# Optimization experiments

Measured on AMD Instinct MI355X. Metric: run time of the kernel, lower is better.

The kernel has to match this reference:

```python
import jax, jax.numpy as jnp
import numpy as np
import math

HIDDEN = 256
HEADS = 8
HEAD_DIM = HIDDEN // HEADS
SCALE = math.sqrt(HEAD_DIM)


def setup_inputs() -> dict:
    key = jax.random.key(0)
    ks = jax.random.split(key, 10)
    B, N = 2, 4096
    x = jax.random.normal(ks[0], (B, N, HIDDEN), dtype=jnp.float32)
    pos = jax.random.normal(ks[1], (B, N, 3), dtype=jnp.float32)
    s = 1.0 / math.sqrt(HIDDEN)
    Wq = jax.random.normal(ks[2], (HIDDEN, HIDDEN), dtype=jnp.float32) * s
    bq = jnp.zeros((HIDDEN,), dtype=jnp.float32)
    Wk = jax.random.normal(ks[3], (HIDDEN, HIDDEN), dtype=jnp.float32) * s
    bk = jnp.zeros((HIDDEN,), dtype=jnp.float32)
    Wv = jax.random.normal(ks[4], (HIDDEN, HIDDEN), dtype=jnp.float32) * s
    bv = jnp.zeros((HIDDEN,), dtype=jnp.float32)
    Wo = jax.random.normal(ks[5], (HIDDEN, HIDDEN), dtype=jnp.float32) * s
    bo = jnp.zeros((HIDDEN,), dtype=jnp.float32)
    return {"x": x, "pos": pos, "Wq": Wq, "bq": bq, "Wk": Wk, "bk": bk,
            "Wv": Wv, "bv": bv, "Wo": Wo, "bo": bo}


def _pairwise_dist(pos):
    # Euclidean cdist via the norm trick; clip for numerical safety.
    sq = jnp.sum(pos * pos, axis=-1)  # [B, N]
    d2 = sq[:, :, None] + sq[:, None, :] - 2.0 * jnp.einsum('bic,bjc->bij', pos, pos)
    return jnp.sqrt(jnp.maximum(d2, 0.0))  # [B, N, N]


def reference(x, pos, Wq, bq, Wk, bk, Wv, bv, Wo, bo):
    B, N, _ = x.shape
    # projections -> [B, H, N, Dh]
    def split_heads(t):
        return t.reshape(B, N, HEADS, HEAD_DIM).transpose(0, 2, 1, 3)
    q = split_heads(x @ Wq.T + bq)
    k = split_heads(x @ Wk.T + bk)
    v = split_heads(x @ Wv.T + bv)
    scores = jnp.einsum('bhid,bhjd->bhij', q, k) / SCALE
    dist_bias = -_pairwise_dist(pos) / 10.0  # [B, N, N]
    scores = scores + dist_bias[:, None, :, :]
    attn = jax.nn.softmax(scores, axis=-1)
    out = jnp.einsum('bhij,bhjd->bhid', attn, v)
    out = out.transpose(0, 2, 1, 3).reshape(B, N, HIDDEN)
    return out @ Wo.T + bo
```

## Files before the change

kernel.cpp:

```cpp
#include <hip/hip_runtime.h>

#define BATCH 2
#define SEQ   4096
#define HID   256
#define NHEAD 8
#define DH    32

typedef __attribute__((ext_vector_type(8))) _Float16 half8;
typedef __attribute__((ext_vector_type(4))) _Float16 half4;
typedef __attribute__((ext_vector_type(4))) float    f32x4;

__global__ void cvt_f32_f16(const float* __restrict__ src,
                            _Float16* __restrict__ dst, int n) {
    int i = (blockIdx.x * blockDim.x + threadIdx.x) * 4;
    if (i >= n) return;
    f32x4 v = *reinterpret_cast<const f32x4*>(src + i);
    half4 h;
#pragma unroll
    for (int c = 0; c < 4; ++c) h[c] = (_Float16)v[c];
    *reinterpret_cast<half4*>(dst + i) = h;
}

__global__ __launch_bounds__(256) void qkv_proj(
    const _Float16* __restrict__ xh, const _Float16* __restrict__ Wh,
    const float* __restrict__ bq, const float* __restrict__ bk,
    const float* __restrict__ bv,
    _Float16* __restrict__ Qh, _Float16* __restrict__ Kh,
    _Float16* __restrict__ Vt)
{
    const int z   = blockIdx.z;
    const int m0  = blockIdx.x * 64;
    const int n0  = blockIdx.y * 64;
    const int tid = threadIdx.x;
    const int w   = tid >> 6, lane = tid & 63;
    const int lr  = lane & 15, lg = lane >> 4;
    const int wr  = (w >> 1) * 32, wc = (w & 1) * 32;

    const _Float16* Wp = Wh + (size_t)z * HID * HID;
    const float* bias = (z == 0) ? bq : (z == 1) ? bk : bv;

    f32x4 acc[2][2] = {};
    const int ar = m0 + wr + lr;
    const int br = n0 + wc + lr;
#pragma unroll
    for (int ks = 0; ks < 8; ++ks) {
        const int ko = ks * 32 + lg * 8;
        half8 a0 = *reinterpret_cast<const half8*>(xh + (size_t)ar * HID + ko);
        half8 a1 = *reinterpret_cast<const half8*>(xh + (size_t)(ar + 16) * HID + ko);
        half8 b0 = *reinterpret_cast<const half8*>(Wp + (size_t)br * HID + ko);
        half8 b1 = *reinterpret_cast<const half8*>(Wp + (size_t)(br + 16) * HID + ko);
        acc[0][0] = __builtin_amdgcn_mfma_f32_16x16x32_f16(a0, b0, acc[0][0], 0, 0, 0);
        acc[0][1] = __builtin_amdgcn_mfma_f32_16x16x32_f16(a0, b1, acc[0][1], 0, 0, 0);
        acc[1][0] = __builtin_amdgcn_mfma_f32_16x16x32_f16(a1, b0, acc[1][0], 0, 0, 0);
        acc[1][1] = __builtin_amdgcn_mfma_f32_16x16x32_f16(a1, b1, acc[1][1], 0, 0, 0);
    }
#pragma unroll
    for (int mf = 0; mf < 2; ++mf)
#pragma unroll
    for (int nf = 0; nf < 2; ++nf)
#pragma unroll
    for (int r = 0; r < 4; ++r) {
        const int m  = m0 + wr + mf * 16 + lg * 4 + r;
        const int o  = n0 + wc + nf * 16 + lr;
        const int bb = m >> 12, nn = m & (SEQ - 1);
        const int hh = o >> 5,  dd = o & (DH - 1);
        float v = acc[mf][nf][r] + bias[o];
        if (z == 0) {
            Qh[(((size_t)(bb * NHEAD + hh) * SEQ) + nn) * DH + dd] =
                (_Float16)(v * 0.17677669529663687f);
        } else if (z == 1) {
            Kh[(((size_t)(bb * NHEAD + hh) * SEQ) + nn) * DH + dd] = (_Float16)v;
        } else {
            Vt[(((size_t)(bb * NHEAD + hh) * DH) + dd) * SEQ + nn] = (_Float16)v;
        }
    }
}

__global__ __launch_bounds__(512) void attn_kernel(
    const _Float16* __restrict__ Qh, const _Float16* __restrict__ Kh,
    const _Float16* __restrict__ Vt, const float* __restrict__ pos,
    _Float16* __restrict__ AO)
{
    __shared__ __align__(16) float pi[32][4];
    __shared__ __align__(16) float pj[64][4];
    __shared__ __align__(16) float sbias[32][68];
    __shared__ __align__(16) _Float16 Pl[NHEAD][2048];

    const int b   = blockIdx.y;
    const int i0  = blockIdx.x * 32;
    const int tid = threadIdx.x;
    const int h   = tid >> 6;
    const int lane = tid & 63;
    const int lr  = lane & 15, lg = lane >> 4;

    if (tid < 32) {
        const float* p = pos + (size_t)(b * SEQ + i0 + tid) * 3;
        float x = p[0], y = p[1], zz = p[2];
        pi[tid][0] = x; pi[tid][1] = y; pi[tid][2] = zz;
        pi[tid][3] = x * x + y * y + zz * zz;
    }

    const _Float16* Qbase = Qh + ((size_t)(b * NHEAD + h) * SEQ + i0) * DH;
    const _Float16* Kbase = Kh + (size_t)(b * NHEAD + h) * SEQ * DH;
    const _Float16* Vbase = Vt + (size_t)(b * NHEAD + h) * DH * SEQ;

    const half8 aq0 = *reinterpret_cast<const half8*>(Qbase + (size_t)lr * DH + lg * 8);
    const half8 aq1 = *reinterpret_cast<const half8*>(Qbase + (size_t)(16 + lr) * DH + lg * 8);

    f32x4 acc[2][2] = {};
    float mrun[2][4], lrun[2][4];
#pragma unroll
    for (int mf = 0; mf < 2; ++mf)
#pragma unroll
    for (int r = 0; r < 4; ++r) { mrun[mf][r] = -__builtin_inff(); lrun[mf][r] = 0.f; }

    char* Pbytes = (char*)&Pl[h][0];

    for (int jt = 0; jt < SEQ / 64; ++jt) {
        const int j0 = jt * 64;
        __syncthreads();
        if (tid < 64) {
            const float* p = pos + (size_t)(b * SEQ + j0 + tid) * 3;
            float x = p[0], y = p[1], zz = p[2];
            pj[tid][0] = x; pj[tid][1] = y; pj[tid][2] = zz;
            pj[tid][3] = x * x + y * y + zz * zz;
        }
        __syncthreads();
        {
            const int row = tid >> 4, c0 = (tid & 15) * 4;
            const float xi = pi[row][0], yi = pi[row][1], zi = pi[row][2], si = pi[row][3];
            f32x4 bb;
#pragma unroll
            for (int c = 0; c < 4; ++c) {
                const int col = c0 + c;
                float dot = xi * pj[col][0] + yi * pj[col][1] + zi * pj[col][2];
                float d2  = si + pj[col][3] - 2.f * dot;
                bb[c] = -0.1f * sqrtf(fmaxf(d2, 0.f));
            }
            *reinterpret_cast<f32x4*>(&sbias[row][c0]) = bb;
        }
        __syncthreads();

        half8 bk8[4];
#pragma unroll
        for (int cf = 0; cf < 4; ++cf)
            bk8[cf] = *reinterpret_cast<const half8*>(
                Kbase + (size_t)(j0 + cf * 16 + lr) * DH + lg * 8);
        f32x4 s[2][4];
#pragma unroll
        for (int mf = 0; mf < 2; ++mf)
#pragma unroll
        for (int cf = 0; cf < 4; ++cf) {
            f32x4 zero = {};
            s[mf][cf] = __builtin_amdgcn_mfma_f32_16x16x32_f16(
                mf ? aq1 : aq0, bk8[cf], zero, 0, 0, 0);
        }

#pragma unroll
        for (int mf = 0; mf < 2; ++mf)
#pragma unroll
        for (int r = 0; r < 4; ++r) {
            const int row = mf * 16 + lg * 4 + r;
            float v[4];
#pragma unroll
            for (int c = 0; c < 4; ++c) v[c] = s[mf][c][r] + sbias[row][c * 16 + lr];
            float tmax = fmaxf(fmaxf(v[0], v[1]), fmaxf(v[2], v[3]));
#pragma unroll
            for (int msk = 8; msk >= 1; msk >>= 1)
                tmax = fmaxf(tmax, __shfl_xor(tmax, msk, 64));
            const float mold = mrun[mf][r];
            const float mnew = fmaxf(mold, tmax);
            const float alpha = __expf(mold - mnew);
            float rsum = 0.f;
#pragma unroll
            for (int c = 0; c < 4; ++c) { v[c] = __expf(v[c] - mnew); rsum += v[c]; }
#pragma unroll
            for (int msk = 8; msk >= 1; msk >>= 1)
                rsum += __shfl_xor(rsum, msk, 64);
            lrun[mf][r] = lrun[mf][r] * alpha + rsum;
            mrun[mf][r] = mnew;
            acc[mf][0][r] *= alpha;
            acc[mf][1][r] *= alpha;
#pragma unroll
            for (int c = 0; c < 4; ++c) {
                const int col = c * 16 + lr;
                const int off = (row * 128 + col * 2) ^ ((row & 7) << 4);
                *reinterpret_cast<_Float16*>(Pbytes + off) = (_Float16)v[c];
            }
        }

#pragma unroll
        for (int ks = 0; ks < 2; ++ks) {
            half8 bv0 = *reinterpret_cast<const half8*>(
                Vbase + (size_t)lr * SEQ + j0 + ks * 32 + lg * 8);
            half8 bv1 = *reinterpret_cast<const half8*>(
                Vbase + (size_t)(16 + lr) * SEQ + j0 + ks * 32 + lg * 8);
#pragma unroll
            for (int mf = 0; mf < 2; ++mf) {
                const int prow = mf * 16 + lr;
                const int poff = (prow * 128 + (ks * 32 + lg * 8) * 2) ^ ((prow & 7) << 4);
                half8 pa = *reinterpret_cast<const half8*>(Pbytes + poff);
                acc[mf][0] = __builtin_amdgcn_mfma_f32_16x16x32_f16(pa, bv0, acc[mf][0], 0, 0, 0);
                acc[mf][1] = __builtin_amdgcn_mfma_f32_16x16x32_f16(pa, bv1, acc[mf][1], 0, 0, 0);
            }
        }
    }

#pragma unroll
    for (int mf = 0; mf < 2; ++mf)
#pragma unroll
    for (int r = 0; r < 4; ++r) {
        const float inv = 1.f / lrun[mf][r];
        const int row = mf * 16 + lg * 4 + r;
#pragma unroll
        for (int df = 0; df < 2; ++df) {
            AO[((size_t)(b * SEQ + i0 + row)) * HID + h * DH + df * 16 + lr] =
                (_Float16)(acc[mf][df][r] * inv);
        }
    }
}

__global__ __launch_bounds__(256) void out_proj(
    const _Float16* __restrict__ AO, const _Float16* __restrict__ Woh,
    const float* __restrict__ bo, float* __restrict__ out)
{
    const int m0  = blockIdx.x * 64;
    const int n0  = blockIdx.y * 64;
    const int tid = threadIdx.x;
    const int w   = tid >> 6, lane = tid & 63;
    const int lr  = lane & 15, lg = lane >> 4;
    const int wr  = (w >> 1) * 32, wc = (w & 1) * 32;

    f32x4 acc[2][2] = {};
    const int ar = m0 + wr + lr;
    const int br = n0 + wc + lr;
#pragma unroll
    for (int ks = 0; ks < 8; ++ks) {
        const int ko = ks * 32 + lg * 8;
        half8 a0 = *reinterpret_cast<const half8*>(AO + (size_t)ar * HID + ko);
        half8 a1 = *reinterpret_cast<const half8*>(AO + (size_t)(ar + 16) * HID + ko);
        half8 b0 = *reinterpret_cast<const half8*>(Woh + (size_t)br * HID + ko);
        half8 b1 = *reinterpret_cast<const half8*>(Woh + (size_t)(br + 16) * HID + ko);
        acc[0][0] = __builtin_amdgcn_mfma_f32_16x16x32_f16(a0, b0, acc[0][0], 0, 0, 0);
        acc[0][1] = __builtin_amdgcn_mfma_f32_16x16x32_f16(a0, b1, acc[0][1], 0, 0, 0);
        acc[1][0] = __builtin_amdgcn_mfma_f32_16x16x32_f16(a1, b0, acc[1][0], 0, 0, 0);
        acc[1][1] = __builtin_amdgcn_mfma_f32_16x16x32_f16(a1, b1, acc[1][1], 0, 0, 0);
    }
#pragma unroll
    for (int mf = 0; mf < 2; ++mf)
#pragma unroll
    for (int nf = 0; nf < 2; ++nf)
#pragma unroll
    for (int r = 0; r < 4; ++r) {
        const int m = m0 + wr + mf * 16 + lg * 4 + r;
        const int o = n0 + wc + nf * 16 + lr;
        out[(size_t)m * HID + o] = acc[mf][nf][r] + bo[o];
    }
}

extern "C" void kernel_launch(void* const* d_in, const int* in_sizes, int n_in,
                              void* d_out, int out_size, void* d_ws, size_t ws_size,
                              hipStream_t stream)
{
    const float* x   = (const float*)d_in[0];
    const float* pos = (const float*)d_in[1];
    const float* Wq  = (const float*)d_in[2];
    const float* bq  = (const float*)d_in[3];
    const float* Wk  = (const float*)d_in[4];
    const float* bk  = (const float*)d_in[5];
    const float* Wv  = (const float*)d_in[6];
    const float* bv  = (const float*)d_in[7];
    const float* Wo  = (const float*)d_in[8];
    const float* bo  = (const float*)d_in[9];
    float* out = (float*)d_out;

    char* ws = (char*)d_ws;
    _Float16* Qh = (_Float16*)(ws);
    _Float16* Kh = (_Float16*)(ws + (4  << 20));
    _Float16* Vt = (_Float16*)(ws + (8  << 20));
    _Float16* xh = (_Float16*)(ws + (12 << 20));
    _Float16* AO = xh;
    _Float16* Wh = (_Float16*)(ws + (16 << 20));

    const int NX = BATCH * SEQ * HID;
    const int NW = HID * HID;
    cvt_f32_f16<<<NX / 1024, 256, 0, stream>>>(x,  xh, NX);
    cvt_f32_f16<<<NW / 1024, 256, 0, stream>>>(Wq, Wh + 0 * NW, NW);
    cvt_f32_f16<<<NW / 1024, 256, 0, stream>>>(Wk, Wh + 1 * NW, NW);
    cvt_f32_f16<<<NW / 1024, 256, 0, stream>>>(Wv, Wh + 2 * NW, NW);
    cvt_f32_f16<<<NW / 1024, 256, 0, stream>>>(Wo, Wh + 3 * NW, NW);

    qkv_proj<<<dim3(BATCH * SEQ / 64, HID / 64, 3), 256, 0, stream>>>(
        xh, Wh, bq, bk, bv, Qh, Kh, Vt);

    attn_kernel<<<dim3(SEQ / 32, BATCH), 512, 0, stream>>>(Qh, Kh, Vt, pos, AO);

    out_proj<<<dim3(BATCH * SEQ / 64, HID / 64), 256, 0, stream>>>(
        AO, Wh + 3 * NW, bo, out);
}
```

Before: 287.8 us.

## Restructure attention: 16-row tiles, exp2 softmax, lazy rescale, fused weight conversion

Rewrites the attention kernel to handle 16 query rows per block and compute the distance bias in 256-column chunks, which cuts the number of block-wide barriers. Softmax switches to exp2 by folding log2(e) into the Q scale and the bias constant, and uses transposed MFMA output so each lane reduces within its own registers. The running max is rescaled only when a tile's max exceeds it by a threshold, skipping most rescales. The four weight conversions are fused into one launch. The tradeoffs are that the bias is now recomputed per 16-row block rather than per 32-row block, and the lazy rescale lets unnormalized values grow up to 2^11.5 before fp16 conversion.

Measured after the change: 235.7 us. 18.1% less time.

```diff
diff --git a/kernel.cpp b/kernel.cpp
--- a/kernel.cpp
+++ b/kernel.cpp
@@ -5,6 +5,9 @@
 #define HID   256
 #define NHEAD 8
 #define DH    32
+#define THR_L2 11.5f
+#define QSCALE 0.25501639769925074f
+#define BIASC (-0.14426950408889634f)
 
 typedef __attribute__((ext_vector_type(8))) _Float16 half8;
 typedef __attribute__((ext_vector_type(4))) _Float16 half4;
@@ -19,6 +22,19 @@
 #pragma unroll
     for (int c = 0; c < 4; ++c) h[c] = (_Float16)v[c];
     *reinterpret_cast<half4*>(dst + i) = h;
+}
+
+__global__ void cvt_w4(const float* __restrict__ a, const float* __restrict__ b,
+                       const float* __restrict__ c, const float* __restrict__ d,
+                       _Float16* __restrict__ dst) {
+    const float* srcs[4] = {a, b, c, d};
+    const float* s = srcs[blockIdx.y];
+    const int i = (blockIdx.x * blockDim.x + threadIdx.x) * 4;
+    f32x4 v = *reinterpret_cast<const f32x4*>(s + i);
+    half4 h;
+#pragma unroll
+    for (int k = 0; k < 4; ++k) h[k] = (_Float16)v[k];
+    *reinterpret_cast<half4*>(dst + (size_t)blockIdx.y * HID * HID + i) = h;
 }
 
 __global__ __launch_bounds__(256) void qkv_proj(
@@ -67,7 +83,7 @@
         float v = acc[mf][nf][r] + bias[o];
         if (z == 0) {
             Qh[(((size_t)(bb * NHEAD + hh) * SEQ) + nn) * DH + dd] =
-                (_Float16)(v * 0.17677669529663687f);
+                (_Float16)(v * QSCALE);
         } else if (z == 1) {
             Kh[(((size_t)(bb * NHEAD + hh) * SEQ) + nn) * DH + dd] = (_Float16)v;
         } else {
@@ -76,147 +92,146 @@
     }
 }
 
-__global__ __launch_bounds__(512) void attn_kernel(
+__global__ __launch_bounds__(512, 4) void attn_kernel(
     const _Float16* __restrict__ Qh, const _Float16* __restrict__ Kh,
     const _Float16* __restrict__ Vt, const float* __restrict__ pos,
     _Float16* __restrict__ AO)
 {
-    __shared__ __align__(16) float pi[32][4];
-    __shared__ __align__(16) float pj[64][4];
-    __shared__ __align__(16) float sbias[32][68];
-    __shared__ __align__(16) _Float16 Pl[NHEAD][2048];
-
-    const int b   = blockIdx.y;
-    const int i0  = blockIdx.x * 32;
-    const int tid = threadIdx.x;
-    const int h   = tid >> 6;
+    __shared__ __align__(16) float pi4[16][4];
+    __shared__ __align__(16) float pj4[256][4];
+    __shared__ __align__(16) float biasL[16][260];
+    __shared__ __align__(16) _Float16 Pl[NHEAD][16 * 72];
+    __shared__ __align__(16) float xposeL[NHEAD][16];
+
+    const int b    = blockIdx.y;
+    const int i0   = blockIdx.x * 16;
+    const int tid  = threadIdx.x;
+    const int w    = tid >> 6;
     const int lane = tid & 63;
-    const int lr  = lane & 15, lg = lane >> 4;
-
-    if (tid < 32) {
+    const int lr   = lane & 15, lg = lane >> 4;
+
+    if (tid < 16) {
         const float* p = pos + (size_t)(b * SEQ + i0 + tid) * 3;
-        float x = p[0], y = p[1], zz = p[2];
-        pi[tid][0] = x; pi[tid][1] = y; pi[tid][2] = zz;
-        pi[tid][3] = x * x + y * y + zz * zz;
-    }
-
-    const _Float16* Qbase = Qh + ((size_t)(b * NHEAD + h) * SEQ + i0) * DH;
-    const _Float16* Kbase = Kh + (size_t)(b * NHEAD + h) * SEQ * DH;
-    const _Float16* Vbase = Vt + (size_t)(b * NHEAD + h) * DH * SEQ;
-
-    const half8 aq0 = *reinterpret_cast<const half8*>(Qbase + (size_t)lr * DH + lg * 8);
-    const half8 aq1 = *reinterpret_cast<const half8*>(Qbase + (size_t)(16 + lr) * DH + lg * 8);
-
-    f32x4 acc[2][2] = {};
-    float mrun[2][4], lrun[2][4];
-#pragma unroll
-    for (int mf = 0; mf < 2; ++mf)
-#pragma unroll
-    for (int r = 0; r < 4; ++r) { mrun[mf][r] = -__builtin_inff(); lrun[mf][r] = 0.f; }
-
-    char* Pbytes = (char*)&Pl[h][0];
-
-    for (int jt = 0; jt < SEQ / 64; ++jt) {
-        const int j0 = jt * 64;
+        float x = p[0], y = p[1], z = p[2];
+        pi4[tid][0] = x; pi4[tid][1] = y; pi4[tid][2] = z;
+        pi4[tid][3] = x * x + y * y + z * z;
+    }
+
+    const size_t bhh = (size_t)(b * NHEAD + w);
+    const _Float16* Qbase = Qh + (bhh * SEQ + i0) * DH;
+    const _Float16* Kbase = Kh + bhh * SEQ * DH;
+    const _Float16* Vbase = Vt + bhh * DH * SEQ;
+
+    const half8 aq = *reinterpret_cast<const half8*>(Qbase + (size_t)lr * DH + lg * 8);
+
+    f32x4 acc0 = {}, acc1 = {};
+    float mrun = -1e30f, lsum = 0.f;
+
+    char* PlW = (char*)&Pl[w][0];
+
+    for (int ch = 0; ch < SEQ / 256; ++ch) {
         __syncthreads();
-        if (tid < 64) {
-            const float* p = pos + (size_t)(b * SEQ + j0 + tid) * 3;
-            float x = p[0], y = p[1], zz = p[2];
-            pj[tid][0] = x; pj[tid][1] = y; pj[tid][2] = zz;
-            pj[tid][3] = x * x + y * y + zz * zz;
+        if (tid < 256) {
+            const float* p = pos + (size_t)(b * SEQ + ch * 256 + tid) * 3;
+            float x = p[0], y = p[1], z = p[2];
+            pj4[tid][0] = x; pj4[tid][1] = y; pj4[tid][2] = z;
+            pj4[tid][3] = x * x + y * y + z * z;
         }
         __syncthreads();
         {
-            const int row = tid >> 4, c0 = (tid & 15) * 4;
-            const float xi = pi[row][0], yi = pi[row][1], zi = pi[row][2], si = pi[row][3];
-            f32x4 bb;
-#pragma unroll
-            for (int c = 0; c < 4; ++c) {
-                const int col = c0 + c;
-                float dot = xi * pj[col][0] + yi * pj[col][1] + zi * pj[col][2];
-                float d2  = si + pj[col][3] - 2.f * dot;
-                bb[c] = -0.1f * sqrtf(fmaxf(d2, 0.f));
-            }
-            *reinterpret_cast<f32x4*>(&sbias[row][c0]) = bb;
+            const int br  = tid & 15;
+            const int c0  = (tid >> 4) * 8;
+            const float xi = pi4[br][0], yi = pi4[br][1], zi = pi4[br][2], si = pi4[br][3];
+            f32x4 o0, o1;
+#pragma unroll
+            for (int k = 0; k < 8; ++k) {
+                const float* pj = &pj4[c0 + k][0];
+                float dot = xi * pj[0] + yi * pj[1] + zi * pj[2];
+                float d2  = si + pj[3] - 2.f * dot;
+                float v   = BIASC * sqrtf(fmaxf(d2, 0.f));
+                if (k < 4) o0[k] = v; else o1[k - 4] = v;
+            }
+            *reinterpret_cast<f32x4*>(&biasL[br][c0])     = o0;
+            *reinterpret_cast<f32x4*>(&biasL[br][c0 + 4]) = o1;
         }
         __syncthreads();
 
-        half8 bk8[4];
-#pragma unroll
-        for (int cf = 0; cf < 4; ++cf)
-            bk8[cf] = *reinterpret_cast<const half8*>(
-                Kbase + (size_t)(j0 + cf * 16 + lr) * DH + lg * 8);
-        f32x4 s[2][4];
-#pragma unroll
-        for (int mf = 0; mf < 2; ++mf)
-#pragma unroll
-        for (int cf = 0; cf < 4; ++cf) {
-            f32x4 zero = {};
-            s[mf][cf] = __builtin_amdgcn_mfma_f32_16x16x32_f16(
-                mf ? aq1 : aq0, bk8[cf], zero, 0, 0, 0);
+        for (int s = 0; s < 4; ++s) {
+            const int j0 = ch * 256 + s * 64;
+
+            half8 k8[4];
+#pragma unroll
+            for (int cf = 0; cf < 4; ++cf)
+                k8[cf] = *reinterpret_cast<const half8*>(
+                    Kbase + (size_t)(j0 + cf * 16 + lr) * DH + lg * 8);
+
+            f32x4 vv[4];
+#pragma unroll
+            for (int cf = 0; cf < 4; ++cf) {
+                f32x4 zero = {};
+                f32x4 sv = __builtin_amdgcn_mfma_f32_16x16x32_f16(k8[cf], aq, zero, 0, 0, 0);
+                f32x4 bb = *reinterpret_cast<const f32x4*>(
+                    &biasL[lr][s * 64 + cf * 16 + lg * 4]);
+                vv[cf] = sv + bb;
+            }
+
+            float tmax = vv[0][0];
+#pragma unroll
+            for (int cf = 0; cf < 4; ++cf)
+#pragma unroll
+            for (int t = 0; t < 4; ++t) tmax = fmaxf(tmax, vv[cf][t]);
+
+            if (!__all(tmax <= mrun + THR_L2)) {
+                float tm = tmax;
+                tm = fmaxf(tm, __shfl_xor(tm, 16, 64));
+                tm = fmaxf(tm, __shfl_xor(tm, 32, 64));
+                const float mnew  = fmaxf(mrun, tm);
+                const float alpha = exp2f(mrun - mnew);
+                if (lane < 16) xposeL[w][lane] = alpha;
+                f32x4 a4 = *reinterpret_cast<const f32x4*>(&xposeL[w][lg * 4]);
+                lsum *= alpha;
+                mrun = mnew;
+                acc0 *= a4;
+                acc1 *= a4;
+            }
+
+#pragma unroll
+            for (int cf = 0; cf < 4; ++cf) {
+                f32x4 p;
+#pragma unroll
+                for (int t = 0; t < 4; ++t) p[t] = exp2f(vv[cf][t] - mrun);
+                lsum += (p[0] + p[1]) + (p[2] + p[3]);
+                half4 hp;
+#pragma unroll
+                for (int t = 0; t < 4; ++t) hp[t] = (_Float16)p[t];
+                *reinterpret_cast<half4*>(
+                    PlW + lr * 144 + (cf * 16 + lg * 4) * 2) = hp;
+            }
+
+#pragma unroll
+            for (int ks = 0; ks < 2; ++ks) {
+                half8 pa = *reinterpret_cast<const half8*>(
+                    PlW + lr * 144 + (ks * 32 + lg * 8) * 2);
+                half8 bv0 = *reinterpret_cast<const half8*>(
+                    Vbase + (size_t)lr * SEQ + j0 + ks * 32 + lg * 8);
+                half8 bv1 = *reinterpret_cast<const half8*>(
+                    Vbase + (size_t)(16 + lr) * SEQ + j0 + ks * 32 + lg * 8);
+                acc0 = __builtin_amdgcn_mfma_f32_16x16x32_f16(pa, bv0, acc0, 0, 0, 0);
+                acc1 = __builtin_amdgcn_mfma_f32_16x16x32_f16(pa, bv1, acc1, 0, 0, 0);
+            }
         }
-
-#pragma unroll
-        for (int mf = 0; mf < 2; ++mf)
-#pragma unroll
-        for (int r = 0; r < 4; ++r) {
-            const int row = mf * 16 + lg * 4 + r;
-            float v[4];
-#pragma unroll
-            for (int c = 0; c < 4; ++c) v[c] = s[mf][c][r] + sbias[row][c * 16 + lr];
-            float tmax = fmaxf(fmaxf(v[0], v[1]), fmaxf(v[2], v[3]));
-#pragma unroll
-            for (int msk = 8; msk >= 1; msk >>= 1)
-                tmax = fmaxf(tmax, __shfl_xor(tmax, msk, 64));
-            const float mold = mrun[mf][r];
-            const float mnew = fmaxf(mold, tmax);
-            const float alpha = __expf(mold - mnew);
-            float rsum = 0.f;
-#pragma unroll
-            for (int c = 0; c < 4; ++c) { v[c] = __expf(v[c] - mnew); rsum += v[c]; }
-#pragma unroll
-            for (int msk = 8; msk >= 1; msk >>= 1)
-                rsum += __shfl_xor(rsum, msk, 64);
-            lrun[mf][r] = lrun[mf][r] * alpha + rsum;
-            mrun[mf][r] = mnew;
-            acc[mf][0][r] *= alpha;
-            acc[mf][1][r] *= alpha;
-#pragma unroll
-            for (int c = 0; c < 4; ++c) {
-                const int col = c * 16 + lr;
-                const int off = (row * 128 + col * 2) ^ ((row & 7) << 4);
-                *reinterpret_cast<_Float16*>(Pbytes + off) = (_Float16)v[c];
-            }
-        }
-
-#pragma unroll
-        for (int ks = 0; ks < 2; ++ks) {
-            half8 bv0 = *reinterpret_cast<const half8*>(
-                Vbase + (size_t)lr * SEQ + j0 + ks * 32 + lg * 8);
-            half8 bv1 = *reinterpret_cast<const half8*>(
-                Vbase + (size_t)(16 + lr) * SEQ + j0 + ks * 32 + lg * 8);
-#pragma unroll
-            for (int mf = 0; mf < 2; ++mf) {
-                const int prow = mf * 16 + lr;
-                const int poff = (prow * 128 + (ks * 32 + lg * 8) * 2) ^ ((prow & 7) << 4);
-                half8 pa = *reinterpret_cast<const half8*>(Pbytes + poff);
-                acc[mf][0] = __builtin_amdgcn_mfma_f32_16x16x32_f16(pa, bv0, acc[mf][0], 0, 0, 0);
-                acc[mf][1] = __builtin_amdgcn_mfma_f32_16x16x32_f16(pa, bv1, acc[mf][1], 0, 0, 0);
-            }
-        }
-    }
-
-#pragma unroll
-    for (int mf = 0; mf < 2; ++mf)
-#pragma unroll
-    for (int r = 0; r < 4; ++r) {
-        const float inv = 1.f / lrun[mf][r];
-        const int row = mf * 16 + lg * 4 + r;
-#pragma unroll
-        for (int df = 0; df < 2; ++df) {
-            AO[((size_t)(b * SEQ + i0 + row)) * HID + h * DH + df * 16 + lr] =
-                (_Float16)(acc[mf][df][r] * inv);
-        }
+    }
+
+    lsum += __shfl_xor(lsum, 16, 64);
+    lsum += __shfl_xor(lsum, 32, 64);
+    const float inv = 1.f / lsum;
+    if (lane < 16) xposeL[w][lane] = inv;
+    f32x4 i4 = *reinterpret_cast<const f32x4*>(&xposeL[w][lg * 4]);
+#pragma unroll
+    for (int t = 0; t < 4; ++t) {
+        const size_t row = (size_t)(b * SEQ + i0 + lg * 4 + t) * HID + w * DH;
+        AO[row + lr]      = (_Float16)(acc0[t] * i4[t]);
+        AO[row + 16 + lr] = (_Float16)(acc1[t] * i4[t]);
     }
 }
 
@@ -284,16 +299,13 @@
 
     const int NX = BATCH * SEQ * HID;
     const int NW = HID * HID;
-    cvt_f32_f16<<<NX / 1024, 256, 0, stream>>>(x,  xh, NX);
-    cvt_f32_f16<<<NW / 1024, 256, 0, stream>>>(Wq, Wh + 0 * NW, NW);
-    cvt_f32_f16<<<NW / 1024, 256, 0, stream>>>(Wk, Wh + 1 * NW, NW);
-    cvt_f32_f16<<<NW / 1024, 256, 0, stream>>>(Wv, Wh + 2 * NW, NW);
-    cvt_f32_f16<<<NW / 1024, 256, 0, stream>>>(Wo, Wh + 3 * NW, NW);
+    cvt_f32_f16<<<NX / 1024, 256, 0, stream>>>(x, xh, NX);
+    cvt_w4<<<dim3(NW / 1024, 4), 256, 0, stream>>>(Wq, Wk, Wv, Wo, Wh);
 
     qkv_proj<<<dim3(BATCH * SEQ / 64, HID / 64, 3), 256, 0, stream>>>(
         xh, Wh, bq, bk, bv, Qh, Kh, Vt);
 
-    attn_kernel<<<dim3(SEQ / 32, BATCH), 512, 0, stream>>>(Qh, Kh, Vt, pos, AO);
+    attn_kernel<<<dim3(SEQ / 16, BATCH), 512, 0, stream>>>(Qh, Kh, Vt, pos, AO);
 
     out_proj<<<dim3(BATCH * SEQ / 64, HID / 64), 256, 0, stream>>>(
         AO, Wh + 3 * NW, bo, out);
```
